# Performance work log

Measured on AMD Instinct MI355X. Metric: run time of the kernel, lower is better.

The kernel has to match this reference:

```python
import jax, jax.numpy as jnp
import numpy as np

HIDDEN = 64

def setup_inputs() -> dict:
    key = jax.random.key(0)
    ks = jax.random.split(key, 10)
    B, E = 8, 200000
    h = jax.random.normal(ks[0], (B, E, HIDDEN), dtype=jnp.float32)
    J = jax.random.normal(ks[1], (B, E, 1), dtype=jnp.float32)
    b_in = jax.random.normal(ks[2], (B, E, 1), dtype=jnp.float32)
    b_out = jax.random.normal(ks[3], (B, E, 1), dtype=jnp.float32)
    d_in = HIDDEN + 4
    # PyTorch Linear default init: U(-1/sqrt(fan_in), 1/sqrt(fan_in))
    def lin(kw, kb, fan_in, fan_out):
        bound = 1.0 / np.sqrt(fan_in)
        W = jax.random.uniform(kw, (fan_in, fan_out), minval=-bound, maxval=bound, dtype=jnp.float32)
        b = jax.random.uniform(kb, (fan_out,), minval=-bound, maxval=bound, dtype=jnp.float32)
        return W, b
    W1, b1 = lin(ks[4], ks[5], d_in, 64)
    W2, b2 = lin(ks[6], ks[7], 64, 64)
    W3, b3 = lin(ks[8], ks[9], 64, 5)
    return {"h": h, "J": J, "b_in": b_in, "b_out": b_out,
            "W1": W1, "b1": b1, "W2": W2, "b2": b2, "W3": W3, "b3": b3}

def reference(h, J, b_in, b_out, W1, b1, W2, b2, W3, b3):
    # concat order matches torch.cat((h, b_in, b_out, J, -J), 2)
    x = jnp.concatenate((h, b_in, b_out, J, -J), axis=2)  # [B,E,hidden+4]
    x = jax.nn.relu(jnp.einsum('bei,io->beo', x, W1) + b1)
    x = jax.nn.relu(jnp.einsum('bei,io->beo', x, W2) + b2)
    message = jnp.einsum('bei,io->beo', x, W3) + b3  # [B,E,5]
    return message
```

## Files before the change

### kernel.cpp

```cpp
#include <hip/hip_runtime.h>

typedef __bf16 bf16x8 __attribute__((ext_vector_type(8)));
typedef float  f32x4  __attribute__((ext_vector_type(4)));

__global__ __launch_bounds__(256, 1)
void msg_mlp(const float* __restrict__ hbuf, const float* __restrict__ Jbuf,
             const float* __restrict__ binb, const float* __restrict__ boutb,
             const float* __restrict__ W1, const float* __restrict__ b1,
             const float* __restrict__ W2, const float* __restrict__ b2,
             const float* __restrict__ W3, const float* __restrict__ b3,
             float* __restrict__ out, int n_rows, int n_tiles)
{
    const int lane = threadIdx.x & 63;
    const int e = lane & 15;
    const int q = lane >> 4;
    const int wid = blockIdx.x * (blockDim.x >> 6) + (threadIdx.x >> 6);
    const int nw  = gridDim.x * (blockDim.x >> 6);

    bf16x8 a1[4][3];
#pragma unroll
    for (int mt = 0; mt < 4; ++mt)
#pragma unroll
      for (int kk = 0; kk < 3; ++kk)
#pragma unroll
        for (int i = 0; i < 8; ++i) {
          const int f = 32*kk + 8*q + i;
          const int o = 16*mt + e;
          float v = 0.0f;
          if (f < 68)       v = W1[f*64 + o];
          else if (f == 68) v = b1[o];
          a1[mt][kk][i] = (__bf16)v;
        }
    bf16x8 a2[4][2];
#pragma unroll
    for (int mt = 0; mt < 4; ++mt)
#pragma unroll
      for (int kk = 0; kk < 2; ++kk)
#pragma unroll
        for (int i = 0; i < 8; ++i) {
          const int f = 16*(2*kk + (i>>2)) + 4*q + (i&3);
          a2[mt][kk][i] = (__bf16)W2[f*64 + 16*mt + e];
        }
    bf16x8 a3[2];
#pragma unroll
    for (int kk = 0; kk < 2; ++kk)
#pragma unroll
      for (int i = 0; i < 8; ++i) {
        const int f = 16*(2*kk + (i>>2)) + 4*q + (i&3);
        a3[kk][i] = (e < 5) ? (__bf16)W3[f*5 + e] : (__bf16)0.0f;
      }
    float b2r[4][4];
#pragma unroll
    for (int mt = 0; mt < 4; ++mt)
#pragma unroll
      for (int r = 0; r < 4; ++r) b2r[mt][r] = b2[16*mt + 4*q + r];
    float b3r[4];
#pragma unroll
    for (int r = 0; r < 4; ++r) b3r[r] = (4*q + r < 5) ? b3[4*q + r] : 0.0f;

    auto issue = [&](int t, f32x4& A, f32x4& Bv, f32x4& C, f32x4& D,
                     float& pin, float& pout, float& pj) {
      int re = t * 16 + e;
      if (re >= n_rows) re = n_rows - 1;
      const float* hr = hbuf + (size_t)re * 64 + 8*q;
      A  = *(const f32x4*)(hr);
      Bv = *(const f32x4*)(hr + 4);
      C  = *(const f32x4*)(hr + 32);
      D  = *(const f32x4*)(hr + 36);
      if (q == 0) { pin = binb[re]; pout = boutb[re]; pj = Jbuf[re]; }
      else        { pin = 0.0f;     pout = 0.0f;      pj = 0.0f; }
    };

    int t = wid;
    f32x4 A0, B0, C0, D0; float p0 = 0.f, q0 = 0.f, j0 = 0.f;
    if (t < n_tiles) issue(t, A0, B0, C0, D0, p0, q0, j0);

    for (; t < n_tiles; t += nw) {
      f32x4 A1, B1, C1, D1; float p1 = 0.f, q1 = 0.f, j1 = 0.f;
      const int tn = t + nw;
      if (tn < n_tiles) issue(tn, A1, B1, C1, D1, p1, q1, j1);

      bf16x8 xb0, xb1, xb2;
#pragma unroll
      for (int i = 0; i < 4; ++i) {
        xb0[i]     = (__bf16)A0[i];
        xb0[i + 4] = (__bf16)B0[i];
        xb1[i]     = (__bf16)C0[i];
        xb1[i + 4] = (__bf16)D0[i];
      }
      xb2[0] = (__bf16)p0; xb2[1] = (__bf16)q0;
      xb2[2] = (__bf16)j0; xb2[3] = (__bf16)(-j0);
      xb2[4] = (q == 0) ? (__bf16)1.0f : (__bf16)0.0f;
      xb2[5] = (__bf16)0.0f; xb2[6] = (__bf16)0.0f; xb2[7] = (__bf16)0.0f;

      f32x4 acc1[4];
#pragma unroll
      for (int mt = 0; mt < 4; ++mt) {
        acc1[mt] = (f32x4){0.f, 0.f, 0.f, 0.f};
        acc1[mt] = __builtin_amdgcn_mfma_f32_16x16x32_bf16(a1[mt][0], xb0, acc1[mt], 0, 0, 0);
        acc1[mt] = __builtin_amdgcn_mfma_f32_16x16x32_bf16(a1[mt][1], xb1, acc1[mt], 0, 0, 0);
        acc1[mt] = __builtin_amdgcn_mfma_f32_16x16x32_bf16(a1[mt][2], xb2, acc1[mt], 0, 0, 0);
      }
      bf16x8 y[2];
#pragma unroll
      for (int kk = 0; kk < 2; ++kk)
#pragma unroll
        for (int i = 0; i < 8; ++i)
          y[kk][i] = (__bf16)fmaxf(acc1[2*kk + (i>>2)][i & 3], 0.0f);

      f32x4 acc2[4];
#pragma unroll
      for (int mt = 0; mt < 4; ++mt) {
        acc2[mt] = (f32x4){b2r[mt][0], b2r[mt][1], b2r[mt][2], b2r[mt][3]};
        acc2[mt] = __builtin_amdgcn_mfma_f32_16x16x32_bf16(a2[mt][0], y[0], acc2[mt], 0, 0, 0);
        acc2[mt] = __builtin_amdgcn_mfma_f32_16x16x32_bf16(a2[mt][1], y[1], acc2[mt], 0, 0, 0);
      }
      bf16x8 z[2];
#pragma unroll
      for (int kk = 0; kk < 2; ++kk)
#pragma unroll
        for (int i = 0; i < 8; ++i)
          z[kk][i] = (__bf16)fmaxf(acc2[2*kk + (i>>2)][i & 3], 0.0f);

      f32x4 acc3 = (f32x4){b3r[0], b3r[1], b3r[2], b3r[3]};
      acc3 = __builtin_amdgcn_mfma_f32_16x16x32_bf16(a3[0], z[0], acc3, 0, 0, 0);
      acc3 = __builtin_amdgcn_mfma_f32_16x16x32_bf16(a3[1], z[1], acc3, 0, 0, 0);

      const int rowi = t * 16 + e;
      if (rowi < n_rows) {
        float* orow = out + (size_t)rowi * 5;
        if (q == 0) {
          orow[0] = acc3[0]; orow[1] = acc3[1];
          orow[2] = acc3[2]; orow[3] = acc3[3];
        } else if (q == 1) {
          orow[4] = acc3[0];
        }
      }

      A0 = A1; B0 = B1; C0 = C1; D0 = D1; p0 = p1; q0 = q1; j0 = j1;
    }
}

extern "C" void kernel_launch(void* const* d_in, const int* in_sizes, int n_in,
                              void* d_out, int out_size, void* d_ws, size_t ws_size,
                              hipStream_t stream) {
    const float* h     = (const float*)d_in[0];
    const float* J     = (const float*)d_in[1];
    const float* b_in  = (const float*)d_in[2];
    const float* b_out = (const float*)d_in[3];
    const float* W1    = (const float*)d_in[4];
    const float* b1    = (const float*)d_in[5];
    const float* W2    = (const float*)d_in[6];
    const float* b2    = (const float*)d_in[7];
    const float* W3    = (const float*)d_in[8];
    const float* b3    = (const float*)d_in[9];
    float* out = (float*)d_out;

    const int n_rows  = in_sizes[1];
    const int n_tiles = (n_rows + 15) / 16;

    dim3 grid(512), block(256);
    hipLaunchKernelGGL(msg_mlp, grid, block, 0, stream,
                       h, J, b_in, b_out, W1, b1, W2, b2, W3, b3,
                       out, n_rows, n_tiles);
}
```

Measured before the change: 97.95 us.

## Process tile pairs per iteration with contiguous loads and folded -J weights

Each wave now handles two 16-row tiles per loop iteration and prefetches the next pair, doubling the loads in flight. Each lane now reads 16 contiguous floats of h and one scalar side input, instead of strided 8-float chunks plus three scalars on lane group 0. The -J term is folded into the weight fragment, which shrinks the K-padding operand. Launch bounds are raised to allow two blocks per CU, but the doubled prefetch registers increase register pressure and could cause spills.

```diff
diff --git a/kernel.cpp b/kernel.cpp
--- a/kernel.cpp
+++ b/kernel.cpp
@@ -3,13 +3,15 @@
 typedef __bf16 bf16x8 __attribute__((ext_vector_type(8)));
 typedef float  f32x4  __attribute__((ext_vector_type(4)));
 
-__global__ __launch_bounds__(256, 1)
+#define MFMA(A, B, C) __builtin_amdgcn_mfma_f32_16x16x32_bf16((A), (B), (C), 0, 0, 0)
+
+__global__ __launch_bounds__(256, 2)
 void msg_mlp(const float* __restrict__ hbuf, const float* __restrict__ Jbuf,
              const float* __restrict__ binb, const float* __restrict__ boutb,
              const float* __restrict__ W1, const float* __restrict__ b1,
              const float* __restrict__ W2, const float* __restrict__ b2,
              const float* __restrict__ W3, const float* __restrict__ b3,
-             float* __restrict__ out, int n_rows, int n_tiles)
+             float* __restrict__ out, int n_rows, int n_pairs)
 {
     const int lane = threadIdx.x & 63;
     const int e = lane & 15;
@@ -17,20 +19,30 @@
     const int wid = blockIdx.x * (blockDim.x >> 6) + (threadIdx.x >> 6);
     const int nw  = gridDim.x * (blockDim.x >> 6);
 
-    bf16x8 a1[4][3];
+    bf16x8 a1[4][2];
 #pragma unroll
     for (int mt = 0; mt < 4; ++mt)
 #pragma unroll
-      for (int kk = 0; kk < 3; ++kk)
+      for (int kk = 0; kk < 2; ++kk)
 #pragma unroll
-        for (int i = 0; i < 8; ++i) {
-          const int f = 32*kk + 8*q + i;
-          const int o = 16*mt + e;
-          float v = 0.0f;
-          if (f < 68)       v = W1[f*64 + o];
-          else if (f == 68) v = b1[o];
-          a1[mt][kk][i] = (__bf16)v;
-        }
+        for (int i = 0; i < 8; ++i)
+          a1[mt][kk][i] = (__bf16)W1[(16*q + 8*kk + i)*64 + 16*mt + e];
+
+    bf16x8 a1x[4];
+#pragma unroll
+    for (int mt = 0; mt < 4; ++mt) {
+      const int o = 16*mt + e;
+      float w0;
+      if      (q == 0) w0 =  W1[64*64 + o];
+      else if (q == 1) w0 =  W1[65*64 + o];
+      else if (q == 2) w0 =  W1[66*64 + o];
+      else             w0 = -W1[67*64 + o];
+      a1x[mt][0] = (__bf16)w0;
+      a1x[mt][1] = (q == 0) ? (__bf16)b1[o] : (__bf16)0.0f;
+#pragma unroll
+      for (int i = 2; i < 8; ++i) a1x[mt][i] = (__bf16)0.0f;
+    }
+
     bf16x8 a2[4][2];
 #pragma unroll
     for (int mt = 0; mt < 4; ++mt)
@@ -58,48 +70,40 @@
 #pragma unroll
     for (int r = 0; r < 4; ++r) b3r[r] = (4*q + r < 5) ? b3[4*q + r] : 0.0f;
 
-    auto issue = [&](int t, f32x4& A, f32x4& Bv, f32x4& C, f32x4& D,
-                     float& pin, float& pout, float& pj) {
-      int re = t * 16 + e;
+    const float* sptr = (q == 0) ? binb : (q == 1) ? boutb : Jbuf;
+    const __bf16 biasf = (q == 0) ? (__bf16)1.0f : (__bf16)0.0f;
+
+    auto issue = [&](int tt, f32x4& h0, f32x4& h1, f32x4& h2, f32x4& h3, float& s) {
+      int re = tt * 16 + e;
       if (re >= n_rows) re = n_rows - 1;
-      const float* hr = hbuf + (size_t)re * 64 + 8*q;
-      A  = *(const f32x4*)(hr);
-      Bv = *(const f32x4*)(hr + 4);
-      C  = *(const f32x4*)(hr + 32);
-      D  = *(const f32x4*)(hr + 36);
-      if (q == 0) { pin = binb[re]; pout = boutb[re]; pj = Jbuf[re]; }
-      else        { pin = 0.0f;     pout = 0.0f;      pj = 0.0f; }
+      const float* hr = hbuf + (size_t)re * 64 + q * 16;
+      h0 = *(const f32x4*)(hr);
+      h1 = *(const f32x4*)(hr + 4);
+      h2 = *(const f32x4*)(hr + 8);
+      h3 = *(const f32x4*)(hr + 12);
+      s = sptr[re];
     };
 
-    int t = wid;
-    f32x4 A0, B0, C0, D0; float p0 = 0.f, q0 = 0.f, j0 = 0.f;
-    if (t < n_tiles) issue(t, A0, B0, C0, D0, p0, q0, j0);
-
-    for (; t < n_tiles; t += nw) {
-      f32x4 A1, B1, C1, D1; float p1 = 0.f, q1 = 0.f, j1 = 0.f;
-      const int tn = t + nw;
-      if (tn < n_tiles) issue(tn, A1, B1, C1, D1, p1, q1, j1);
-
+    auto compute_store = [&](f32x4 h0, f32x4 h1, f32x4 h2, f32x4 h3, float s, int tt) {
       bf16x8 xb0, xb1, xb2;
 #pragma unroll
       for (int i = 0; i < 4; ++i) {
-        xb0[i]     = (__bf16)A0[i];
-        xb0[i + 4] = (__bf16)B0[i];
-        xb1[i]     = (__bf16)C0[i];
-        xb1[i + 4] = (__bf16)D0[i];
+        xb0[i]     = (__bf16)h0[i];
+        xb0[i + 4] = (__bf16)h1[i];
+        xb1[i]     = (__bf16)h2[i];
+        xb1[i + 4] = (__bf16)h3[i];
       }
-      xb2[0] = (__bf16)p0; xb2[1] = (__bf16)q0;
-      xb2[2] = (__bf16)j0; xb2[3] = (__bf16)(-j0);
-      xb2[4] = (q == 0) ? (__bf16)1.0f : (__bf16)0.0f;
-      xb2[5] = (__bf16)0.0f; xb2[6] = (__bf16)0.0f; xb2[7] = (__bf16)0.0f;
+      xb2[0] = (__bf16)s; xb2[1] = biasf;
+#pragma unroll
+      for (int i = 2; i < 8; ++i) xb2[i] = (__bf16)0.0f;
 
       f32x4 acc1[4];
 #pragma unroll
       for (int mt = 0; mt < 4; ++mt) {
         acc1[mt] = (f32x4){0.f, 0.f, 0.f, 0.f};
-        acc1[mt] = __builtin_amdgcn_mfma_f32_16x16x32_bf16(a1[mt][0], xb0, acc1[mt], 0, 0, 0);
-        acc1[mt] = __builtin_amdgcn_mfma_f32_16x16x32_bf16(a1[mt][1], xb1, acc1[mt], 0, 0, 0);
-        acc1[mt] = __builtin_amdgcn_mfma_f32_16x16x32_bf16(a1[mt][2], xb2, acc1[mt], 0, 0, 0);
+        acc1[mt] = MFMA(a1[mt][0], xb0, acc1[mt]);
+        acc1[mt] = MFMA(a1[mt][1], xb1, acc1[mt]);
+        acc1[mt] = MFMA(a1x[mt],   xb2, acc1[mt]);
       }
       bf16x8 y[2];
 #pragma unroll
@@ -112,8 +116,8 @@
 #pragma unroll
       for (int mt = 0; mt < 4; ++mt) {
         acc2[mt] = (f32x4){b2r[mt][0], b2r[mt][1], b2r[mt][2], b2r[mt][3]};
-        acc2[mt] = __builtin_amdgcn_mfma_f32_16x16x32_bf16(a2[mt][0], y[0], acc2[mt], 0, 0, 0);
-        acc2[mt] = __builtin_amdgcn_mfma_f32_16x16x32_bf16(a2[mt][1], y[1], acc2[mt], 0, 0, 0);
+        acc2[mt] = MFMA(a2[mt][0], y[0], acc2[mt]);
+        acc2[mt] = MFMA(a2[mt][1], y[1], acc2[mt]);
       }
       bf16x8 z[2];
 #pragma unroll
@@ -123,10 +127,10 @@
           z[kk][i] = (__bf16)fmaxf(acc2[2*kk + (i>>2)][i & 3], 0.0f);
 
       f32x4 acc3 = (f32x4){b3r[0], b3r[1], b3r[2], b3r[3]};
-      acc3 = __builtin_amdgcn_mfma_f32_16x16x32_bf16(a3[0], z[0], acc3, 0, 0, 0);
-      acc3 = __builtin_amdgcn_mfma_f32_16x16x32_bf16(a3[1], z[1], acc3, 0, 0, 0);
+      acc3 = MFMA(a3[0], z[0], acc3);
+      acc3 = MFMA(a3[1], z[1], acc3);
 
-      const int rowi = t * 16 + e;
+      const int rowi = tt * 16 + e;
       if (rowi < n_rows) {
         float* orow = out + (size_t)rowi * 5;
         if (q == 0) {
@@ -136,8 +140,30 @@
           orow[4] = acc3[0];
         }
       }
+    };
 
-      A0 = A1; B0 = B1; C0 = C1; D0 = D1; p0 = p1; q0 = q1; j0 = j1;
+    int p = wid;
+    f32x4 c00, c01, c02, c03, c10, c11, c12, c13;
+    float s0 = 0.f, s1 = 0.f;
+    if (p < n_pairs) {
+      issue(2*p,     c00, c01, c02, c03, s0);
+      issue(2*p + 1, c10, c11, c12, c13, s1);
+    }
+
+    for (; p < n_pairs; p += nw) {
+      f32x4 n00, n01, n02, n03, n10, n11, n12, n13;
+      float t0 = 0.f, t1 = 0.f;
+      const int pn = p + nw;
+      if (pn < n_pairs) {
+        issue(2*pn,     n00, n01, n02, n03, t0);
+        issue(2*pn + 1, n10, n11, n12, n13, t1);
+      }
+
+      compute_store(c00, c01, c02, c03, s0, 2*p);
+      compute_store(c10, c11, c12, c13, s1, 2*p + 1);
+
+      c00 = n00; c01 = n01; c02 = n02; c03 = n03; s0 = t0;
+      c10 = n10; c11 = n11; c12 = n12; c13 = n13; s1 = t1;
     }
 }
 
@@ -157,10 +183,10 @@
     float* out = (float*)d_out;
 
     const int n_rows  = in_sizes[1];
-    const int n_tiles = (n_rows + 15) / 16;
+    const int n_pairs = (n_rows + 31) / 32;
 
     dim3 grid(512), block(256);
     hipLaunchKernelGGL(msg_mlp, grid, block, 0, stream,
                        h, J, b_in, b_out, W1, b1, W2, b2, W3, b3,
-                       out, n_rows, n_tiles);
+                       out, n_rows, n_pairs);
 }
```

Result: slower. 103.1 us (+5.2%).
